# Performance work log

Measured on AMD Instinct MI355X. Metric: run time of the kernel, lower is better.

## Reference

```python
import jax, jax.numpy as jnp
import numpy as np

HEADS, HID, OUT_C, IN_C = 8, 128, 2, 64
D = HID // HEADS
NODE = {"cell0": 50000, "cell1": 100000, "cell2": 25000}
# (src_type, dst_type, edge_name, num_edges)
ETYPES = [("cell0", "cell0", "u00", 200000),
          ("cell1", "cell1", "u11", 200000),
          ("cell1", "cell0", "b10", 100000),
          ("cell2", "cell1", "b21", 50000)]


def _segment_softmax(scores, seg, num_segments):
    # numerically-stable softmax over irregular destination segments
    m = jax.ops.segment_max(scores, seg, num_segments=num_segments)
    e = jnp.exp(scores - m[seg])
    s = jax.ops.segment_sum(e, seg, num_segments=num_segments)
    return e / (s[seg] + 1e-16)


def setup_inputs() -> dict:
    key = jax.random.key(0)
    ks = iter(jax.random.split(key, 64))
    s = 0.1
    inp = {}
    for nt, n in NODE.items():
        inp[f"x_{nt}"] = jax.random.normal(next(ks), (n, IN_C), jnp.float32)
    for st, dt, name, e in ETYPES:
        src = jax.random.randint(next(ks), (e,), 0, NODE[st], jnp.int32)
        dst = jax.random.randint(next(ks), (e,), 0, NODE[dt], jnp.int32)
        inp[f"ei_{name}"] = jnp.stack([src, dst])
    # HANConv params: per node-type projection, per edge-type attention vectors
    for nt in NODE:
        inp[f"W_{nt}"] = jax.random.normal(next(ks), (IN_C, HID), jnp.float32) * s
        inp[f"b_{nt}"] = jnp.zeros((HID,), jnp.float32)
    for _, _, name, _ in ETYPES:
        inp[f"as_{name}"] = jax.random.normal(next(ks), (HEADS, D), jnp.float32) * s
        inp[f"ad_{name}"] = jax.random.normal(next(ks), (HEADS, D), jnp.float32) * s
    # semantic attention params + final classifier
    inp["k_w"] = jax.random.normal(next(ks), (HID, HID), jnp.float32) * s
    inp["k_b"] = jnp.zeros((HID,), jnp.float32)
    inp["q"] = jax.random.normal(next(ks), (HID,), jnp.float32) * s
    inp["lin_w"] = jax.random.normal(next(ks), (HID, OUT_C), jnp.float32) * s
    inp["lin_b"] = jnp.zeros((OUT_C,), jnp.float32)
    return inp


def _han_conv(x, ei, W, b, att_s, att_d, k_w, k_b, q):
    # node-level: project each node type -> [N, H, D]
    h = {nt: (x[nt] @ W[nt] + b[nt]).reshape(-1, HEADS, D) for nt in NODE}
    outs = {nt: [] for nt in NODE}
    for st, dt, name, _ in ETYPES:
        xs, xd = h[st], h[dt]
        a_s = (xs * att_s[name]).sum(-1)  # [Ns, H]
        a_d = (xd * att_d[name]).sum(-1)  # [Nd, H]
        src, dst = ei[name][0], ei[name][1]
        alpha = jax.nn.leaky_relu(a_s[src] + a_d[dst], 0.2)  # [E, H]
        alpha = _segment_softmax(alpha, dst, NODE[dt])
        msg = xs[src] * alpha[:, :, None]  # [E, H, D]
        agg = jax.ops.segment_sum(msg, dst, num_segments=NODE[dt])
        outs[dt].append(jax.nn.relu(agg.reshape(-1, HID)))
    # semantic-level attention across metapaths per dst node type
    res = {}
    for nt, lst in outs.items():
        if not lst:
            res[nt] = None
            continue
        stk = jnp.stack(lst)  # [M, N, HID]
        score = (q * jnp.tanh(stk @ k_w + k_b).mean(1)).sum(-1)  # [M]
        attn = jax.nn.softmax(score)
        res[nt] = jnp.einsum('m,mnf->nf', attn, stk)
    return res


def reference(x_cell0, x_cell1, x_cell2,
              W_cell0, b_cell0, W_cell1, b_cell1, W_cell2, b_cell2,
              as_u00, ad_u00, as_u11, ad_u11, as_b10, ad_b10, as_b21, ad_b21,
              k_w, k_b, q, lin_w, lin_b,
              ei_u00, ei_u11, ei_b10, ei_b21):
    x = {"cell0": x_cell0, "cell1": x_cell1, "cell2": x_cell2}
    ei = {"u00": ei_u00, "u11": ei_u11, "b10": ei_b10, "b21": ei_b21}
    W = {"cell0": W_cell0, "cell1": W_cell1, "cell2": W_cell2}
    b = {"cell0": b_cell0, "cell1": b_cell1, "cell2": b_cell2}
    att_s = {"u00": as_u00, "u11": as_u11, "b10": as_b10, "b21": as_b21}
    att_d = {"u00": ad_u00, "u11": ad_u11, "b10": ad_b10, "b21": ad_b21}
    # HAN.forward calls han_conv twice with identical inputs (first result
    # discarded); in eval mode (dropout off) both calls are identical math,
    # so we compute it once.
    out = _han_conv(x, ei, W, b, att_s, att_d, k_w, k_b, q)
    pooled = sum(jnp.sum(v, axis=0) for v in out.values() if v is not None)  # global_add_pool, batch=None
    return jax.nn.sigmoid(pooled[None, :] @ lin_w + lin_b)  # [1, OUT_C]
```

## Files before the change

### kernel.cpp

```cpp
#include <hip/hip_runtime.h>
#include <hip/hip_fp16.h>

#define N0 50000
#define N1 100000
#define N2 25000
#define E00 200000
#define E11 200000
#define E10 100000
#define E21 50000
#define EE  550000
#define ND  300000
#define NB  293
#define NT_ALL 18750
#define HID 128
#define INC 64

typedef _Float16 half8 __attribute__((ext_vector_type(8)));
typedef _Float16 half4_t __attribute__((ext_vector_type(4)));
typedef float float4v __attribute__((ext_vector_type(4)));
typedef float floatx2 __attribute__((ext_vector_type(2)));

struct PrepT {
    const float* W; const float* bias;
    const float* av0; const float* av1; const float* av2; const float* av3;
    _Float16* wtg; _Float16* adtg; float* bdc;
};

__global__ __launch_bounds__(256) void prep_kernel(
    PrepT p0, PrepT p1, PrepT p2,
    const float* __restrict__ kw, const float* __restrict__ lw,
    unsigned char* __restrict__ kwf8)
{
    if (blockIdx.x >= 24) {
        int base = (blockIdx.x - 24) * 256 + threadIdx.x;
        for (int it = 0; it < 9; ++it) {
            int idx = base + it * 2048;
            int f = idx >> 7, g = idx & 127;
            float v;
            if (f < 128)      v = kw[g * 128 + f];
            else if (f < 130) v = lw[g * 2 + (f - 128)];
            else              v = 0.f;
            int r = __builtin_amdgcn_cvt_pk_fp8_f32(v, 0.f, 0, false);
            kwf8[idx] = (unsigned char)r;
        }
        return;
    }
    PrepT P = (blockIdx.x >= 16) ? p2 : (blockIdx.x >= 8) ? p1 : p0;
    const int lb = blockIdx.x & 7;
    const int t2 = lb * 256 + threadIdx.x;

    {
        int f = t2 >> 4, g0 = (t2 & 15) * 4;
        half4_t v;
#pragma unroll
        for (int j = 0; j < 4; ++j) v[j] = (_Float16)P.W[(g0 + j) * 128 + f];
        *(half4_t*)&P.wtg[f * 64 + g0] = v;
    }
    {
        int c = t2 >> 6, g = t2 & 63;
        const float* av = (c < 8) ? P.av0 : (c < 16) ? P.av1 : (c < 24) ? P.av2 : P.av3;
        float v = 0.f;
        if (av) {
            int hh = c & 7;
#pragma unroll
            for (int d = 0; d < 16; ++d)
                v += P.W[g * 128 + hh * 16 + d] * av[hh * 16 + d];
        }
        P.adtg[c * 64 + g] = (_Float16)v;
    }
    if (lb == 0 && threadIdx.x < 32) {
        int c = threadIdx.x;
        const float* av = (c < 8) ? P.av0 : (c < 16) ? P.av1 : (c < 24) ? P.av2 : P.av3;
        float v = 0.f;
        if (av) {
            int hh = c & 7;
#pragma unroll
            for (int d = 0; d < 16; ++d)
                v += P.bias[hh * 16 + d] * av[hh * 16 + d];
        }
        P.bdc[c] = v;
    }
}

struct PT {
    const float* x; const float* bias; unsigned char* h;
    float* ao0; float* ao1; float* ao2; float* ao3;
    const _Float16* wtg; const _Float16* adtg; const float* bdc;
    int N; int ntiles; int bstart; int nblocks;
};

#define HPAD 136

__global__ __launch_bounds__(256, 2) void proj_mfma(PT t0, PT t1, PT t2)
{
    __shared__ _Float16 ht[4][16][HPAD];
    const int tid = threadIdx.x;
    const int lane = tid & 63, wv = tid >> 6;
    const int fi = lane & 15, hi = lane >> 4;

    PT A = (blockIdx.x >= t2.bstart) ? t2 : (blockIdx.x >= t1.bstart) ? t1 : t0;

    half8 bfr[8][2], bd[2][2];
#pragma unroll
    for (int nt = 0; nt < 8; ++nt)
#pragma unroll
        for (int kb = 0; kb < 2; ++kb)
            bfr[nt][kb] = *(const half8*)&A.wtg[(nt * 16 + fi) * 64 + kb * 32 + hi * 8];
#pragma unroll
    for (int t = 0; t < 2; ++t)
#pragma unroll
        for (int kb = 0; kb < 2; ++kb)
            bd[t][kb] = *(const half8*)&A.adtg[(t * 16 + fi) * 64 + kb * 32 + hi * 8];

    float bvv[8];
#pragma unroll
    for (int nt = 0; nt < 8; ++nt) bvv[nt] = A.bias[nt * 16 + fi];
    const float bdc0 = A.bdc[fi];
    const float bdc1 = A.bdc[16 + fi];

    float* aolo = (fi >= 8) ? A.ao1 : A.ao0;
    float* aohi = (fi >= 8) ? A.ao3 : A.ao2;
    const bool has_hi = (A.ao2 != nullptr) || (A.ao3 != nullptr);

    const int stride = A.nblocks * 4;
    for (int t = (blockIdx.x - A.bstart) * 4 + wv; t < A.ntiles; t += stride) {
        const int base = t * 16;
        int rsrc = base + fi; if (rsrc >= A.N) rsrc = A.N - 1;
        const float* xp = A.x + (size_t)rsrc * 64 + hi * 8;
        float4 u0 = *(const float4*)(xp);
        float4 u1 = *(const float4*)(xp + 4);
        float4 u2 = *(const float4*)(xp + 32);
        float4 u3 = *(const float4*)(xp + 36);
        half8 a0, a1;
        a0[0] = (_Float16)u0.x; a0[1] = (_Float16)u0.y; a0[2] = (_Float16)u0.z; a0[3] = (_Float16)u0.w;
        a0[4] = (_Float16)u1.x; a0[5] = (_Float16)u1.y; a0[6] = (_Float16)u1.z; a0[7] = (_Float16)u1.w;
        a1[0] = (_Float16)u2.x; a1[1] = (_Float16)u2.y; a1[2] = (_Float16)u2.z; a1[3] = (_Float16)u2.w;
        a1[4] = (_Float16)u3.x; a1[5] = (_Float16)u3.y; a1[6] = (_Float16)u3.z; a1[7] = (_Float16)u3.w;

        float4v c[8];
#pragma unroll
        for (int nt = 0; nt < 8; ++nt) {
            float4v z = {0.f, 0.f, 0.f, 0.f};
            z = __builtin_amdgcn_mfma_f32_16x16x32_f16(a0, bfr[nt][0], z, 0, 0, 0);
            z = __builtin_amdgcn_mfma_f32_16x16x32_f16(a1, bfr[nt][1], z, 0, 0, 0);
            c[nt] = z;
        }
        float4v d0 = {0.f, 0.f, 0.f, 0.f};
        d0 = __builtin_amdgcn_mfma_f32_16x16x32_f16(a0, bd[0][0], d0, 0, 0, 0);
        d0 = __builtin_amdgcn_mfma_f32_16x16x32_f16(a1, bd[0][1], d0, 0, 0, 0);
        float4v d1 = {0.f, 0.f, 0.f, 0.f};
        if (has_hi) {
            d1 = __builtin_amdgcn_mfma_f32_16x16x32_f16(a0, bd[1][0], d1, 0, 0, 0);
            d1 = __builtin_amdgcn_mfma_f32_16x16x32_f16(a1, bd[1][1], d1, 0, 0, 0);
        }

#pragma unroll
        for (int nt = 0; nt < 8; ++nt)
#pragma unroll
            for (int r = 0; r < 4; ++r)
                ht[wv][hi * 4 + r][nt * 16 + fi] = (_Float16)(c[nt][r] + bvv[nt]);
#pragma unroll
        for (int i = 0; i < 4; ++i) {
            int row = i * 4 + hi;
            int node = base + row;
            if (node < A.N) {
                half8 v = *(const half8*)&ht[wv][row][fi * 8];
                int pa = __builtin_amdgcn_cvt_pk_fp8_f32((float)v[0], (float)v[1], 0, false);
                pa = __builtin_amdgcn_cvt_pk_fp8_f32((float)v[2], (float)v[3], pa, true);
                int pb = __builtin_amdgcn_cvt_pk_fp8_f32((float)v[4], (float)v[5], 0, false);
                pb = __builtin_amdgcn_cvt_pk_fp8_f32((float)v[6], (float)v[7], pb, true);
                int2 o = {pa, pb};
                *(int2*)(A.h + (size_t)node * 128 + fi * 8) = o;
            }
        }
        if (aolo) {
#pragma unroll
            for (int r = 0; r < 4; ++r) {
                int node = base + hi * 4 + r;
                if (node < A.N) aolo[(size_t)node * 8 + (fi & 7)] = d0[r] + bdc0;
            }
        }
        if (aohi) {
#pragma unroll
            for (int r = 0; r < 4; ++r) {
                int node = base + hi * 4 + r;
                if (node < A.N) aohi[(size_t)node * 8 + (fi & 7)] = d1[r] + bdc1;
            }
        }
    }
}

__device__ __forceinline__ void decode_edge(
    int e, const int* ei00, const int* ei10, const int* ei11, const int* ei21,
    int& src, int& slot)
{
    if (e < E00)                    { src = ei00[e];               slot = ei00[E00 + e]; }
    else if (e < E00 + E10)         { int i = e - E00;             src = ei10[i]; slot = 50000  + ei10[E10 + i]; }
    else if (e < E00 + E10 + E11)   { int i = e - E00 - E10;       src = ei11[i]; slot = 100000 + ei11[E11 + i]; }
    else                            { int i = e - E00 - E10 - E11; src = ei21[i]; slot = 200000 + ei21[E21 + i]; }
}

__global__ __launch_bounds__(256) void count_kernel(
    const int* __restrict__ ei00, const int* __restrict__ ei10,
    const int* __restrict__ ei11, const int* __restrict__ ei21,
    int* __restrict__ cnt)
{
    int e = blockIdx.x * 256 + threadIdx.x;
    if (e >= EE) return;
    int src, slot;
    decode_edge(e, ei00, ei10, ei11, ei21, src, slot);
    atomicAdd(&cnt[slot], 1);
}

__global__ __launch_bounds__(256) void scan1_kernel(
    const int* __restrict__ cnt, int* __restrict__ part)
{
    const int tid = threadIdx.x, b = blockIdx.x;
    int i0 = b * 1024 + tid * 4;
    int s = 0;
#pragma unroll
    for (int k = 0; k < 4; ++k) { int i = i0 + k; s += (i < ND) ? cnt[i] : 0; }
#pragma unroll
    for (int off = 1; off < 64; off <<= 1) s += __shfl_xor(s, off);
    __shared__ int wt[4];
    if ((tid & 63) == 0) wt[tid >> 6] = s;
    __syncthreads();
    if (tid == 0) part[b] = wt[0] + wt[1] + wt[2] + wt[3];
}

__global__ __launch_bounds__(256) void scan2_kernel(int* __restrict__ part)
{
    const int t = threadIdx.x;
    int p0 = (2 * t     < NB) ? part[2 * t]     : 0;
    int p1 = (2 * t + 1 < NB) ? part[2 * t + 1] : 0;
    int ps = p0 + p1;
    __shared__ int sd[256];
    sd[t] = ps; __syncthreads();
    for (int d = 1; d < 256; d <<= 1) {
        int v = (t >= d) ? sd[t - d] : 0;
        __syncthreads();
        sd[t] += v;
        __syncthreads();
    }
    int exc = sd[t] - ps;
    if (2 * t     < NB) part[2 * t]     = exc;
    if (2 * t + 1 < NB) part[2 * t + 1] = exc + p0;
}

__global__ __launch_bounds__(256) void scan3_kernel(
    const int* __restrict__ cnt, const int* __restrict__ part,
    int* __restrict__ off, int* __restrict__ cursor)
{
    const int tid = threadIdx.x, b = blockIdx.x;
    const int lane = tid & 63, wv = tid >> 6;
    int i0 = b * 1024 + tid * 4;
    int v[4];
#pragma unroll
    for (int k = 0; k < 4; ++k) { int i = i0 + k; v[k] = (i < ND) ? cnt[i] : 0; }
    int ts = v[0] + v[1] + v[2] + v[3];
    int inc = ts;
#pragma unroll
    for (int d = 1; d < 64; d <<= 1) {
        int u = __shfl_up(inc, d);
        if (lane >= d) inc += u;
    }
    int wexc = inc - ts;
    __shared__ int wt[4];
    if (lane == 63) wt[wv] = inc;
    __syncthreads();
    int wbase = 0;
    for (int w = 0; w < wv; ++w) wbase += wt[w];
    int base = part[b] + wbase + wexc;
    int pre = 0;
#pragma unroll
    for (int k = 0; k < 4; ++k) {
        int i = i0 + k;
        if (i < ND) { off[i] = base + pre; cursor[i] = base + pre; }
        pre += v[k];
    }
}

__global__ __launch_bounds__(256) void fill_kernel(
    const int* __restrict__ ei00, const int* __restrict__ ei10,
    const int* __restrict__ ei11, const int* __restrict__ ei21,
    const float* __restrict__ as00, const float* __restrict__ ad00,
    const float* __restrict__ as10, const float* __restrict__ ad10,
    const float* __restrict__ as11, const float* __restrict__ ad11,
    const float* __restrict__ as21, const float* __restrict__ ad21,
    int* __restrict__ cursor, int* __restrict__ srcs, _Float16* __restrict__ wgt)
{
    int e = blockIdx.x * 256 + threadIdx.x;
    if (e >= EE) return;
    int src, d, slot;
    const float* asp; const float* adp;
    if (e < E00) {
        src = ei00[e]; d = ei00[E00 + e]; slot = d; asp = as00; adp = ad00;
    } else if (e < E00 + E10) {
        int i = e - E00; src = ei10[i]; d = ei10[E10 + i]; slot = 50000 + d; asp = as10; adp = ad10;
    } else if (e < E00 + E10 + E11) {
        int i = e - E00 - E10; src = ei11[i]; d = ei11[E11 + i]; slot = 100000 + d; asp = as11; adp = ad11;
    } else {
        int i = e - E00 - E10 - E11; src = ei21[i]; d = ei21[E21 + i]; slot = 200000 + d; asp = as21; adp = ad21;
    }
    float4 sa0 = *(const float4*)(asp + (size_t)src * 8);
    float4 sa1 = *(const float4*)(asp + (size_t)src * 8 + 4);
    float4 da0 = *(const float4*)(adp + (size_t)d * 8);
    float4 da1 = *(const float4*)(adp + (size_t)d * 8 + 4);
    float vv[8] = {sa0.x + da0.x, sa0.y + da0.y, sa0.z + da0.z, sa0.w + da0.w,
                   sa1.x + da1.x, sa1.y + da1.y, sa1.z + da1.z, sa1.w + da1.w};
    half8 w;
#pragma unroll
    for (int h = 0; h < 8; ++h) {
        float v = vv[h];
        v = v > 0.f ? v : 0.2f * v;
        w[h] = (_Float16)__expf(v);
    }
    int pos = atomicAdd(&cursor[slot], 1);
    srcs[pos] = src;
    *(half8*)(wgt + (size_t)pos * 8) = w;
}

__global__ __launch_bounds__(256) void gather_kernel(
    const int* __restrict__ cnt, const int* __restrict__ off,
    const int* __restrict__ srcs, const _Float16* __restrict__ wgt,
    const unsigned char* __restrict__ h0, const unsigned char* __restrict__ h1,
    const unsigned char* __restrict__ h2,
    unsigned char* __restrict__ agg)
{
    const int gid = blockIdx.x * 256 + threadIdx.x;
    const int lane = gid & 63;
    const int grp = lane >> 4, lg = lane & 15;
    const int slot = (gid >> 6) * 4 + grp;
    const int head = lg >> 1;
    const unsigned char* hs = (slot < 50000) ? h0 : (slot < 200000) ? h1 : h2;
    const int deg = cnt[slot], st = off[slot];

    int degm = deg;
    degm = max(degm, __shfl_xor(degm, 16));
    degm = max(degm, __shfl_xor(degm, 32));

    float acc[8] = {0.f, 0.f, 0.f, 0.f, 0.f, 0.f, 0.f, 0.f};
    float sw = 0.f;
    int i = 0;
    for (; i + 2 <= degm; i += 2) {
        bool a0 = (i < deg), a1 = (i + 1 < deg);
        int s0 = 0, s1 = 0;
        if (a0) s0 = srcs[st + i];
        if (a1) s1 = srcs[st + i + 1];
        float w0 = 0.f, w1 = 0.f;
        unsigned long long v0 = 0, v1 = 0;
        if (a0) { w0 = (float)wgt[(size_t)(st + i) * 8 + head];
                  v0 = *(const unsigned long long*)(hs + (size_t)s0 * 128 + lg * 8); }
        if (a1) { w1 = (float)wgt[(size_t)(st + i + 1) * 8 + head];
                  v1 = *(const unsigned long long*)(hs + (size_t)s1 * 128 + lg * 8); }
        int l0 = (int)(v0 & 0xffffffffu), m0 = (int)(v0 >> 32);
        int l1 = (int)(v1 & 0xffffffffu), m1 = (int)(v1 >> 32);
        floatx2 f0a = __builtin_amdgcn_cvt_pk_f32_fp8(l0, false);
        floatx2 f0b = __builtin_amdgcn_cvt_pk_f32_fp8(l0, true);
        floatx2 f0c = __builtin_amdgcn_cvt_pk_f32_fp8(m0, false);
        floatx2 f0d = __builtin_amdgcn_cvt_pk_f32_fp8(m0, true);
        floatx2 f1a = __builtin_amdgcn_cvt_pk_f32_fp8(l1, false);
        floatx2 f1b = __builtin_amdgcn_cvt_pk_f32_fp8(l1, true);
        floatx2 f1c = __builtin_amdgcn_cvt_pk_f32_fp8(m1, false);
        floatx2 f1d = __builtin_amdgcn_cvt_pk_f32_fp8(m1, true);
        acc[0] += w0 * f0a.x + w1 * f1a.x;
        acc[1] += w0 * f0a.y + w1 * f1a.y;
        acc[2] += w0 * f0b.x + w1 * f1b.x;
        acc[3] += w0 * f0b.y + w1 * f1b.y;
        acc[4] += w0 * f0c.x + w1 * f1c.x;
        acc[5] += w0 * f0c.y + w1 * f1c.y;
        acc[6] += w0 * f0d.x + w1 * f1d.x;
        acc[7] += w0 * f0d.y + w1 * f1d.y;
        sw += w0 + w1;
    }
    if (i < degm) {
        bool a0 = (i < deg);
        int s0 = 0;
        if (a0) s0 = srcs[st + i];
        float w0 = 0.f;
        unsigned long long v0 = 0;
        if (a0) { w0 = (float)wgt[(size_t)(st + i) * 8 + head];
                  v0 = *(const unsigned long long*)(hs + (size_t)s0 * 128 + lg * 8); }
        int l0 = (int)(v0 & 0xffffffffu), m0 = (int)(v0 >> 32);
        floatx2 f0a = __builtin_amdgcn_cvt_pk_f32_fp8(l0, false);
        floatx2 f0b = __builtin_amdgcn_cvt_pk_f32_fp8(l0, true);
        floatx2 f0c = __builtin_amdgcn_cvt_pk_f32_fp8(m0, false);
        floatx2 f0d = __builtin_amdgcn_cvt_pk_f32_fp8(m0, true);
        acc[0] += w0 * f0a.x; acc[1] += w0 * f0a.y;
        acc[2] += w0 * f0b.x; acc[3] += w0 * f0b.y;
        acc[4] += w0 * f0c.x; acc[5] += w0 * f0c.y;
        acc[6] += w0 * f0d.x; acc[7] += w0 * f0d.y;
        sw += w0;
    }

    float rr = __builtin_amdgcn_rcpf(sw + 1e-16f);
    float r[8];
#pragma unroll
    for (int j = 0; j < 8; ++j) r[j] = fmaxf(acc[j] * rr, 0.f);
    int pa = __builtin_amdgcn_cvt_pk_fp8_f32(r[0], r[1], 0, false);
    pa = __builtin_amdgcn_cvt_pk_fp8_f32(r[2], r[3], pa, true);
    int pb = __builtin_amdgcn_cvt_pk_fp8_f32(r[4], r[5], 0, false);
    pb = __builtin_amdgcn_cvt_pk_fp8_f32(r[6], r[7], pb, true);
    int2 o = {pa, pb};
    *(int2*)(agg + (size_t)slot * 128 + lg * 8) = o;
}

__global__ __launch_bounds__(256, 2) void semantic_kernel(
    const unsigned char* __restrict__ agg, const unsigned char* __restrict__ kwf8,
    const float* __restrict__ kb, const float* __restrict__ q,
    float* __restrict__ cs2, float* __restrict__ score)
{
    __shared__ float redv[12];
    const int tid = threadIdx.x;
    const int lane = tid & 63, wv = tid >> 6;
    const int fi = lane & 15, hi = lane >> 4;

    if (tid < 12) redv[tid] = 0.f;
    __syncthreads();

    long bf[9][4];
#pragma unroll
    for (int ft = 0; ft < 9; ++ft)
#pragma unroll
        for (int kk = 0; kk < 4; ++kk)
            bf[ft][kk] = *(const long*)&kwf8[(ft * 16 + fi) * 128 + kk * 32 + hi * 8];

    float qv[8], kbv[8];
#pragma unroll
    for (int ft = 0; ft < 8; ++ft) {
        qv[ft] = q[ft * 16 + fi];
        kbv[ft] = kb[ft * 16 + fi];
    }

    float sc[4] = {0.f, 0.f, 0.f, 0.f};
    float cs[4] = {0.f, 0.f, 0.f, 0.f};
    const int wid = blockIdx.x * 4 + wv;
    const int nw = gridDim.x * 4;

    long af[4] = {0, 0, 0, 0};
    int t = wid;
    if (t < NT_ALL) {
        const unsigned char* rowp = agg + ((size_t)(t * 16 + fi) * 128 + hi * 8);
        af[0] = *(const long*)(rowp);
        af[1] = *(const long*)(rowp + 32);
        af[2] = *(const long*)(rowp + 64);
        af[3] = *(const long*)(rowp + 96);
    }
    while (t < NT_ALL) {
        const int tn = t + nw;
        long afn[4] = {0, 0, 0, 0};
        if (tn < NT_ALL) {
            const unsigned char* rowp = agg + ((size_t)(tn * 16 + fi) * 128 + hi * 8);
            afn[0] = *(const long*)(rowp);
            afn[1] = *(const long*)(rowp + 32);
            afn[2] = *(const long*)(rowp + 64);
            afn[3] = *(const long*)(rowp + 96);
        }
        const int m = (t >= 12500) ? 3 : (t >= 6250) ? 2 : (t >= 3125) ? 1 : 0;
        float tsc = 0.f, tcs;
#pragma unroll
        for (int ft = 0; ft < 8; ++ft) {
            float4v c = {0.f, 0.f, 0.f, 0.f};
            c = __builtin_amdgcn_mfma_f32_16x16x32_fp8_fp8(af[0], bf[ft][0], c, 0, 0, 0);
            c = __builtin_amdgcn_mfma_f32_16x16x32_fp8_fp8(af[1], bf[ft][1], c, 0, 0, 0);
            c = __builtin_amdgcn_mfma_f32_16x16x32_fp8_fp8(af[2], bf[ft][2], c, 0, 0, 0);
            c = __builtin_amdgcn_mfma_f32_16x16x32_fp8_fp8(af[3], bf[ft][3], c, 0, 0, 0);
#pragma unroll
            for (int r = 0; r < 4; ++r) {
                float y = c[r] + kbv[ft];
                float e = __expf(2.f * y);
                tsc += qv[ft] * (1.f - 2.f * __builtin_amdgcn_rcpf(e + 1.f));
            }
        }
        {
            float4v c = {0.f, 0.f, 0.f, 0.f};
            c = __builtin_amdgcn_mfma_f32_16x16x32_fp8_fp8(af[0], bf[8][0], c, 0, 0, 0);
            c = __builtin_amdgcn_mfma_f32_16x16x32_fp8_fp8(af[1], bf[8][1], c, 0, 0, 0);
            c = __builtin_amdgcn_mfma_f32_16x16x32_fp8_fp8(af[2], bf[8][2], c, 0, 0, 0);
            c = __builtin_amdgcn_mfma_f32_16x16x32_fp8_fp8(af[3], bf[8][3], c, 0, 0, 0);
            tcs = c[0] + c[1] + c[2] + c[3];
        }
        if (m == 0)      { sc[0] += tsc; cs[0] += tcs; }
        else if (m == 1) { sc[1] += tsc; cs[1] += tcs; }
        else if (m == 2) { sc[2] += tsc; cs[2] += tcs; }
        else             { sc[3] += tsc; cs[3] += tcs; }
        t = tn;
        af[0] = afn[0]; af[1] = afn[1]; af[2] = afn[2]; af[3] = afn[3];
    }

#pragma unroll
    for (int m = 0; m < 4; ++m) {
        float s = sc[m];
#pragma unroll
        for (int off = 1; off < 64; off <<= 1) s += __shfl_xor(s, off);
        if (lane == 0 && s != 0.f) atomicAdd(&redv[m], s);
        float v = cs[m];
        v += __shfl_xor(v, 16);
        v += __shfl_xor(v, 32);
        if (hi == 0 && fi < 2 && v != 0.f) atomicAdd(&redv[4 + 2 * m + fi], v);
    }
    __syncthreads();
    if (tid < 4)              atomicAdd(&score[tid], redv[tid]);
    if (tid >= 4 && tid < 12) atomicAdd(&cs2[tid - 4], redv[tid]);
}

__global__ void final_kernel(const float* __restrict__ cs2,
                             const float* __restrict__ score,
                             const float* __restrict__ lb,
                             float* __restrict__ out)
{
    float s0 = score[0] / (float)N0;
    float s1 = score[1] / (float)N0;
    float s2 = score[2] / (float)N1;
    float s3 = score[3] / (float)N1;
    float m0 = fmaxf(s0, s1);
    float e0 = expf(s0 - m0), e1 = expf(s1 - m0);
    float a0 = e0 / (e0 + e1), a1 = e1 / (e0 + e1);
    float m1 = fmaxf(s2, s3);
    float e2 = expf(s2 - m1), e3 = expf(s3 - m1);
    float a2 = e2 / (e2 + e3), a3 = e3 / (e2 + e3);
    float z0 = a0 * cs2[0] + a1 * cs2[2] + a2 * cs2[4] + a3 * cs2[6] + lb[0];
    float z1 = a0 * cs2[1] + a1 * cs2[3] + a2 * cs2[5] + a3 * cs2[7] + lb[1];
    out[0] = 1.f / (1.f + expf(-z0));
    out[1] = 1.f / (1.f + expf(-z1));
}

extern "C" void kernel_launch(void* const* d_in, const int* in_sizes, int n_in,
                              void* d_out, int out_size, void* d_ws, size_t ws_size,
                              hipStream_t stream)
{
    const float* x0  = (const float*)d_in[0];
    const float* x1  = (const float*)d_in[1];
    const float* x2  = (const float*)d_in[2];
    const int* ei00  = (const int*)d_in[3];
    const int* ei11  = (const int*)d_in[4];
    const int* ei10  = (const int*)d_in[5];
    const int* ei21  = (const int*)d_in[6];
    const float* W0  = (const float*)d_in[7];  const float* b0 = (const float*)d_in[8];
    const float* W1  = (const float*)d_in[9];  const float* b1 = (const float*)d_in[10];
    const float* W2  = (const float*)d_in[11]; const float* b2 = (const float*)d_in[12];
    const float* as00 = (const float*)d_in[13]; const float* ad00 = (const float*)d_in[14];
    const float* as11 = (const float*)d_in[15]; const float* ad11 = (const float*)d_in[16];
    const float* as10 = (const float*)d_in[17]; const float* ad10 = (const float*)d_in[18];
    const float* as21 = (const float*)d_in[19]; const float* ad21 = (const float*)d_in[20];
    const float* kw  = (const float*)d_in[21]; const float* kb  = (const float*)d_in[22];
    const float* q   = (const float*)d_in[23];
    const float* lw  = (const float*)d_in[24]; const float* lb  = (const float*)d_in[25];
    float* out = (float*)d_out;

    char* p = (char*)d_ws;
    auto alloc = [&](size_t bytes) {
        char* r = p;
        p += (bytes + 255) & ~(size_t)255;
        return r;
    };
    unsigned char* h0 = (unsigned char*)alloc((size_t)N0 * 128);
    unsigned char* h1 = (unsigned char*)alloc((size_t)N1 * 128);
    unsigned char* h2 = (unsigned char*)alloc((size_t)N2 * 128);
    float* o_as00 = (float*)alloc((size_t)N0 * 32);
    float* o_ad00 = (float*)alloc((size_t)N0 * 32);
    float* o_as11 = (float*)alloc((size_t)N1 * 32);
    float* o_ad11 = (float*)alloc((size_t)N1 * 32);
    float* o_as10 = (float*)alloc((size_t)N1 * 32);
    float* o_ad10 = (float*)alloc((size_t)N0 * 32);
    float* o_as21 = (float*)alloc((size_t)N2 * 32);
    float* o_ad21 = (float*)alloc((size_t)N1 * 32);
    int* off    = (int*)alloc((size_t)ND * 4);
    int* cursor = (int*)alloc((size_t)ND * 4);
    int* part   = (int*)alloc((size_t)512 * 4);
    int* srcs   = (int*)alloc((size_t)EE * 4);
    _Float16* wgt = (_Float16*)alloc((size_t)EE * 16);
    unsigned char* agg = (unsigned char*)alloc((size_t)ND * 128);
    _Float16* wtg0 = (_Float16*)alloc(128 * 64 * 2);
    _Float16* wtg1 = (_Float16*)alloc(128 * 64 * 2);
    _Float16* wtg2 = (_Float16*)alloc(128 * 64 * 2);
    _Float16* adtg0 = (_Float16*)alloc(32 * 64 * 2);
    _Float16* adtg1 = (_Float16*)alloc(32 * 64 * 2);
    _Float16* adtg2 = (_Float16*)alloc(32 * 64 * 2);
    float* bdcg = (float*)alloc(3 * 32 * 4);
    unsigned char* kwf8 = (unsigned char*)alloc(144 * 128);
    char* zstart = p;
    int* cnt = (int*)alloc((size_t)ND * 4);
    float* colsum2 = (float*)alloc(8 * 4);
    float* score   = (float*)alloc(4 * 4);
    size_t zbytes = (size_t)(p - zstart);

    (void)hipMemsetAsync(zstart, 0, zbytes, stream);

    PrepT pp0 = {W0, b0, as00, ad00, ad10, nullptr, wtg0, adtg0, bdcg + 0};
    PrepT pp1 = {W1, b1, as11, ad11, as10, ad21,    wtg1, adtg1, bdcg + 32};
    PrepT pp2 = {W2, b2, as21, nullptr, nullptr, nullptr, wtg2, adtg2, bdcg + 64};
    prep_kernel<<<32, 256, 0, stream>>>(pp0, pp1, pp2, kw, lw, kwf8);

    PT t0 = {x0, b0, h0,
             o_as00, o_ad00, o_ad10, nullptr,
             wtg0, adtg0, bdcg + 0,
             N0, 3125, 0, 296};
    PT t1 = {x1, b1, h1,
             o_as11, o_ad11, o_as10, o_ad21,
             wtg1, adtg1, bdcg + 32,
             N1, 6250, 296, 584};
    PT t2 = {x2, b2, h2,
             o_as21, nullptr, nullptr, nullptr,
             wtg2, adtg2, bdcg + 64,
             N2, 1563, 880, 144};
    proj_mfma<<<1024, 256, 0, stream>>>(t0, t1, t2);

    count_kernel<<<(EE + 255) / 256, 256, 0, stream>>>(ei00, ei10, ei11, ei21, cnt);
    scan1_kernel<<<NB, 256, 0, stream>>>(cnt, part);
    scan2_kernel<<<1, 256, 0, stream>>>(part);
    scan3_kernel<<<NB, 256, 0, stream>>>(cnt, part, off, cursor);
    fill_kernel<<<(EE + 255) / 256, 256, 0, stream>>>(ei00, ei10, ei11, ei21,
        o_as00, o_ad00, o_as10, o_ad10, o_as11, o_ad11, o_as21, o_ad21,
        cursor, srcs, wgt);

    gather_kernel<<<ND / 16, 256, 0, stream>>>(cnt, off, srcs, wgt, h0, h1, h2, agg);

    semantic_kernel<<<1024, 256, 0, stream>>>(agg, kwf8, kb, q, colsum2, score);

    final_kernel<<<1, 1, 0, stream>>>(colsum2, score, lb, out);
}
```

Baseline: 289.3 us.

## Fuse CSR build launches into neighbors and widen gather to 16-byte rows

Result: faster. 283.1 us (-2.2%).

```diff
diff --git a/kernel.cpp b/kernel.cpp
--- a/kernel.cpp
+++ b/kernel.cpp
@@ -26,11 +26,32 @@
     _Float16* wtg; _Float16* adtg; float* bdc;
 };
 
+__device__ __forceinline__ void decode_edge(
+    int e, const int* ei00, const int* ei10, const int* ei11, const int* ei21,
+    int& src, int& slot)
+{
+    if (e < E00)                    { src = ei00[e];               slot = ei00[E00 + e]; }
+    else if (e < E00 + E10)         { int i = e - E00;             src = ei10[i]; slot = 50000  + ei10[E10 + i]; }
+    else if (e < E00 + E10 + E11)   { int i = e - E00 - E10;       src = ei11[i]; slot = 100000 + ei11[E11 + i]; }
+    else                            { int i = e - E00 - E10 - E11; src = ei21[i]; slot = 200000 + ei21[E21 + i]; }
+}
+
 __global__ __launch_bounds__(256) void prep_kernel(
     PrepT p0, PrepT p1, PrepT p2,
     const float* __restrict__ kw, const float* __restrict__ lw,
-    unsigned char* __restrict__ kwf8)
-{
+    unsigned char* __restrict__ kwf8,
+    const int* __restrict__ ei00, const int* __restrict__ ei10,
+    const int* __restrict__ ei11, const int* __restrict__ ei21,
+    int* __restrict__ cnt)
+{
+    if (blockIdx.x >= 32) {
+        int e = (blockIdx.x - 32) * 256 + threadIdx.x;
+        if (e >= EE) return;
+        int src, slot;
+        decode_edge(e, ei00, ei10, ei11, ei21, src, slot);
+        atomicAdd(&cnt[slot], 1);
+        return;
+    }
     if (blockIdx.x >= 24) {
         int base = (blockIdx.x - 24) * 256 + threadIdx.x;
         for (int it = 0; it < 9; ++it) {
@@ -48,7 +69,6 @@
     PrepT P = (blockIdx.x >= 16) ? p2 : (blockIdx.x >= 8) ? p1 : p0;
     const int lb = blockIdx.x & 7;
     const int t2 = lb * 256 + threadIdx.x;
-
     {
         int f = t2 >> 4, g0 = (t2 & 15) * 4;
         half4_t v;
@@ -90,13 +110,31 @@
 };
 
 #define HPAD 136
-
-__global__ __launch_bounds__(256, 2) void proj_mfma(PT t0, PT t1, PT t2)
+#define PROJ_BLKS 1024
+
+__global__ __launch_bounds__(256, 2) void proj_mfma(
+    PT t0, PT t1, PT t2,
+    const int* __restrict__ cnt, int* __restrict__ part)
 {
     __shared__ _Float16 ht[4][16][HPAD];
+    __shared__ int swt[4];
     const int tid = threadIdx.x;
     const int lane = tid & 63, wv = tid >> 6;
     const int fi = lane & 15, hi = lane >> 4;
+
+    if (blockIdx.x >= PROJ_BLKS) {
+        const int b = blockIdx.x - PROJ_BLKS;
+        int i0 = b * 1024 + tid * 4;
+        int s = 0;
+#pragma unroll
+        for (int k = 0; k < 4; ++k) { int i = i0 + k; s += (i < ND) ? cnt[i] : 0; }
+#pragma unroll
+        for (int off = 1; off < 64; off <<= 1) s += __shfl_xor(s, off);
+        if ((tid & 63) == 0) swt[tid >> 6] = s;
+        __syncthreads();
+        if (tid == 0) part[b] = swt[0] + swt[1] + swt[2] + swt[3];
+        return;
+    }
 
     PT A = (blockIdx.x >= t2.bstart) ? t2 : (blockIdx.x >= t1.bstart) ? t1 : t0;
 
@@ -190,69 +228,31 @@
     }
 }
 
-__device__ __forceinline__ void decode_edge(
-    int e, const int* ei00, const int* ei10, const int* ei11, const int* ei21,
-    int& src, int& slot)
-{
-    if (e < E00)                    { src = ei00[e];               slot = ei00[E00 + e]; }
-    else if (e < E00 + E10)         { int i = e - E00;             src = ei10[i]; slot = 50000  + ei10[E10 + i]; }
-    else if (e < E00 + E10 + E11)   { int i = e - E00 - E10;       src = ei11[i]; slot = 100000 + ei11[E11 + i]; }
-    else                            { int i = e - E00 - E10 - E11; src = ei21[i]; slot = 200000 + ei21[E21 + i]; }
-}
-
-__global__ __launch_bounds__(256) void count_kernel(
-    const int* __restrict__ ei00, const int* __restrict__ ei10,
-    const int* __restrict__ ei11, const int* __restrict__ ei21,
-    int* __restrict__ cnt)
-{
-    int e = blockIdx.x * 256 + threadIdx.x;
-    if (e >= EE) return;
-    int src, slot;
-    decode_edge(e, ei00, ei10, ei11, ei21, src, slot);
-    atomicAdd(&cnt[slot], 1);
-}
-
-__global__ __launch_bounds__(256) void scan1_kernel(
-    const int* __restrict__ cnt, int* __restrict__ part)
-{
-    const int tid = threadIdx.x, b = blockIdx.x;
-    int i0 = b * 1024 + tid * 4;
-    int s = 0;
-#pragma unroll
-    for (int k = 0; k < 4; ++k) { int i = i0 + k; s += (i < ND) ? cnt[i] : 0; }
-#pragma unroll
-    for (int off = 1; off < 64; off <<= 1) s += __shfl_xor(s, off);
-    __shared__ int wt[4];
-    if ((tid & 63) == 0) wt[tid >> 6] = s;
-    __syncthreads();
-    if (tid == 0) part[b] = wt[0] + wt[1] + wt[2] + wt[3];
-}
-
-__global__ __launch_bounds__(256) void scan2_kernel(int* __restrict__ part)
-{
-    const int t = threadIdx.x;
-    int p0 = (2 * t     < NB) ? part[2 * t]     : 0;
-    int p1 = (2 * t + 1 < NB) ? part[2 * t + 1] : 0;
-    int ps = p0 + p1;
-    __shared__ int sd[256];
-    sd[t] = ps; __syncthreads();
-    for (int d = 1; d < 256; d <<= 1) {
-        int v = (t >= d) ? sd[t - d] : 0;
-        __syncthreads();
-        sd[t] += v;
-        __syncthreads();
-    }
-    int exc = sd[t] - ps;
-    if (2 * t     < NB) part[2 * t]     = exc;
-    if (2 * t + 1 < NB) part[2 * t + 1] = exc + p0;
-}
-
-__global__ __launch_bounds__(256) void scan3_kernel(
+__global__ __launch_bounds__(256) void scan23_kernel(
     const int* __restrict__ cnt, const int* __restrict__ part,
     int* __restrict__ off, int* __restrict__ cursor)
 {
+    __shared__ int sd[256];
+    __shared__ int pex[512];
+    __shared__ int wt[4];
     const int tid = threadIdx.x, b = blockIdx.x;
     const int lane = tid & 63, wv = tid >> 6;
+
+    int p0 = (2 * tid     < NB) ? part[2 * tid]     : 0;
+    int p1 = (2 * tid + 1 < NB) ? part[2 * tid + 1] : 0;
+    int ps = p0 + p1;
+    sd[tid] = ps; __syncthreads();
+    for (int d = 1; d < 256; d <<= 1) {
+        int v = (tid >= d) ? sd[tid - d] : 0;
+        __syncthreads();
+        sd[tid] += v;
+        __syncthreads();
+    }
+    int exc = sd[tid] - ps;
+    pex[2 * tid] = exc;
+    pex[2 * tid + 1] = exc + p0;
+    __syncthreads();
+
     int i0 = b * 1024 + tid * 4;
     int v[4];
 #pragma unroll
@@ -265,12 +265,11 @@
         if (lane >= d) inc += u;
     }
     int wexc = inc - ts;
-    __shared__ int wt[4];
     if (lane == 63) wt[wv] = inc;
     __syncthreads();
     int wbase = 0;
     for (int w = 0; w < wv; ++w) wbase += wt[w];
-    int base = part[b] + wbase + wexc;
+    int base = pex[b] + wbase + wexc;
     int pre = 0;
 #pragma unroll
     for (int k = 0; k < 4; ++k) {
@@ -329,18 +328,21 @@
 {
     const int gid = blockIdx.x * 256 + threadIdx.x;
     const int lane = gid & 63;
-    const int grp = lane >> 4, lg = lane & 15;
-    const int slot = (gid >> 6) * 4 + grp;
-    const int head = lg >> 1;
+    const int g8 = lane >> 3, sub = lane & 7;
+    const int slot = (gid >> 6) * 8 + g8;
     const unsigned char* hs = (slot < 50000) ? h0 : (slot < 200000) ? h1 : h2;
     const int deg = cnt[slot], st = off[slot];
 
     int degm = deg;
+    degm = max(degm, __shfl_xor(degm, 8));
     degm = max(degm, __shfl_xor(degm, 16));
     degm = max(degm, __shfl_xor(degm, 32));
 
-    float acc[8] = {0.f, 0.f, 0.f, 0.f, 0.f, 0.f, 0.f, 0.f};
+    float acc[16];
+#pragma unroll
+    for (int j = 0; j < 16; ++j) acc[j] = 0.f;
     float sw = 0.f;
+
     int i = 0;
     for (; i + 2 <= degm; i += 2) {
         bool a0 = (i < deg), a1 = (i + 1 < deg);
@@ -348,29 +350,24 @@
         if (a0) s0 = srcs[st + i];
         if (a1) s1 = srcs[st + i + 1];
         float w0 = 0.f, w1 = 0.f;
-        unsigned long long v0 = 0, v1 = 0;
-        if (a0) { w0 = (float)wgt[(size_t)(st + i) * 8 + head];
-                  v0 = *(const unsigned long long*)(hs + (size_t)s0 * 128 + lg * 8); }
-        if (a1) { w1 = (float)wgt[(size_t)(st + i + 1) * 8 + head];
-                  v1 = *(const unsigned long long*)(hs + (size_t)s1 * 128 + lg * 8); }
-        int l0 = (int)(v0 & 0xffffffffu), m0 = (int)(v0 >> 32);
-        int l1 = (int)(v1 & 0xffffffffu), m1 = (int)(v1 >> 32);
-        floatx2 f0a = __builtin_amdgcn_cvt_pk_f32_fp8(l0, false);
-        floatx2 f0b = __builtin_amdgcn_cvt_pk_f32_fp8(l0, true);
-        floatx2 f0c = __builtin_amdgcn_cvt_pk_f32_fp8(m0, false);
-        floatx2 f0d = __builtin_amdgcn_cvt_pk_f32_fp8(m0, true);
-        floatx2 f1a = __builtin_amdgcn_cvt_pk_f32_fp8(l1, false);
-        floatx2 f1b = __builtin_amdgcn_cvt_pk_f32_fp8(l1, true);
-        floatx2 f1c = __builtin_amdgcn_cvt_pk_f32_fp8(m1, false);
-        floatx2 f1d = __builtin_amdgcn_cvt_pk_f32_fp8(m1, true);
-        acc[0] += w0 * f0a.x + w1 * f1a.x;
-        acc[1] += w0 * f0a.y + w1 * f1a.y;
-        acc[2] += w0 * f0b.x + w1 * f1b.x;
-        acc[3] += w0 * f0b.y + w1 * f1b.y;
-        acc[4] += w0 * f0c.x + w1 * f1c.x;
-        acc[5] += w0 * f0c.y + w1 * f1c.y;
-        acc[6] += w0 * f0d.x + w1 * f1d.x;
-        acc[7] += w0 * f0d.y + w1 * f1d.y;
+        int4 v0 = {0, 0, 0, 0}, v1 = {0, 0, 0, 0};
+        if (a0) { w0 = (float)wgt[(size_t)(st + i) * 8 + sub];
+                  v0 = *(const int4*)(hs + (size_t)s0 * 128 + sub * 16); }
+        if (a1) { w1 = (float)wgt[(size_t)(st + i + 1) * 8 + sub];
+                  v1 = *(const int4*)(hs + (size_t)s1 * 128 + sub * 16); }
+        const int wa[4] = {v0.x, v0.y, v0.z, v0.w};
+        const int wb[4] = {v1.x, v1.y, v1.z, v1.w};
+#pragma unroll
+        for (int k = 0; k < 4; ++k) {
+            floatx2 fa0 = __builtin_amdgcn_cvt_pk_f32_fp8(wa[k], false);
+            floatx2 fa1 = __builtin_amdgcn_cvt_pk_f32_fp8(wa[k], true);
+            floatx2 fb0 = __builtin_amdgcn_cvt_pk_f32_fp8(wb[k], false);
+            floatx2 fb1 = __builtin_amdgcn_cvt_pk_f32_fp8(wb[k], true);
+            acc[4 * k + 0] += w0 * fa0.x + w1 * fb0.x;
+            acc[4 * k + 1] += w0 * fa0.y + w1 * fb0.y;
+            acc[4 * k + 2] += w0 * fa1.x + w1 * fb1.x;
+            acc[4 * k + 3] += w0 * fa1.y + w1 * fb1.y;
+        }
         sw += w0 + w1;
     }
     if (i < degm) {
@@ -378,37 +375,45 @@
         int s0 = 0;
         if (a0) s0 = srcs[st + i];
         float w0 = 0.f;
-        unsigned long long v0 = 0;
-        if (a0) { w0 = (float)wgt[(size_t)(st + i) * 8 + head];
-                  v0 = *(const unsigned long long*)(hs + (size_t)s0 * 128 + lg * 8); }
-        int l0 = (int)(v0 & 0xffffffffu), m0 = (int)(v0 >> 32);
-        floatx2 f0a = __builtin_amdgcn_cvt_pk_f32_fp8(l0, false);
-        floatx2 f0b = __builtin_amdgcn_cvt_pk_f32_fp8(l0, true);
-        floatx2 f0c = __builtin_amdgcn_cvt_pk_f32_fp8(m0, false);
-        floatx2 f0d = __builtin_amdgcn_cvt_pk_f32_fp8(m0, true);
-        acc[0] += w0 * f0a.x; acc[1] += w0 * f0a.y;
-        acc[2] += w0 * f0b.x; acc[3] += w0 * f0b.y;
-        acc[4] += w0 * f0c.x; acc[5] += w0 * f0c.y;
-        acc[6] += w0 * f0d.x; acc[7] += w0 * f0d.y;
+        int4 v0 = {0, 0, 0, 0};
+        if (a0) { w0 = (float)wgt[(size_t)(st + i) * 8 + sub];
+                  v0 = *(const int4*)(hs + (size_t)s0 * 128 + sub * 16); }
+        const int wa[4] = {v0.x, v0.y, v0.z, v0.w};
+#pragma unroll
+        for (int k = 0; k < 4; ++k) {
+            floatx2 fa0 = __builtin_amdgcn_cvt_pk_f32_fp8(wa[k], false);
+            floatx2 fa1 = __builtin_amdgcn_cvt_pk_f32_fp8(wa[k], true);
+            acc[4 * k + 0] += w0 * fa0.x;
+            acc[4 * k + 1] += w0 * fa0.y;
+            acc[4 * k + 2] += w0 * fa1.x;
+            acc[4 * k + 3] += w0 * fa1.y;
+        }
         sw += w0;
     }
 
     float rr = __builtin_amdgcn_rcpf(sw + 1e-16f);
-    float r[8];
-#pragma unroll
-    for (int j = 0; j < 8; ++j) r[j] = fmaxf(acc[j] * rr, 0.f);
-    int pa = __builtin_amdgcn_cvt_pk_fp8_f32(r[0], r[1], 0, false);
-    pa = __builtin_amdgcn_cvt_pk_fp8_f32(r[2], r[3], pa, true);
-    int pb = __builtin_amdgcn_cvt_pk_fp8_f32(r[4], r[5], 0, false);
-    pb = __builtin_amdgcn_cvt_pk_fp8_f32(r[6], r[7], pb, true);
-    int2 o = {pa, pb};
-    *(int2*)(agg + (size_t)slot * 128 + lg * 8) = o;
+    int4 o;
+    int pk[4];
+#pragma unroll
+    for (int k = 0; k < 4; ++k) {
+        float r0 = fmaxf(acc[4 * k + 0] * rr, 0.f);
+        float r1 = fmaxf(acc[4 * k + 1] * rr, 0.f);
+        float r2 = fmaxf(acc[4 * k + 2] * rr, 0.f);
+        float r3 = fmaxf(acc[4 * k + 3] * rr, 0.f);
+        int p = __builtin_amdgcn_cvt_pk_fp8_f32(r0, r1, 0, false);
+        p = __builtin_amdgcn_cvt_pk_fp8_f32(r2, r3, p, true);
+        pk[k] = p;
+    }
+    o.x = pk[0]; o.y = pk[1]; o.z = pk[2]; o.w = pk[3];
+    *(int4*)(agg + (size_t)slot * 128 + sub * 16) = o;
 }
 
 __global__ __launch_bounds__(256, 2) void semantic_kernel(
     const unsigned char* __restrict__ agg, const unsigned char* __restrict__ kwf8,
     const float* __restrict__ kb, const float* __restrict__ q,
-    float* __restrict__ cs2, float* __restrict__ score)
+    const float* __restrict__ lb,
+    float* __restrict__ cs2, float* __restrict__ score,
+    unsigned int* __restrict__ done, float* __restrict__ out)
 {
     __shared__ float redv[12];
     const int tid = threadIdx.x;
@@ -502,27 +507,29 @@
     __syncthreads();
     if (tid < 4)              atomicAdd(&score[tid], redv[tid]);
     if (tid >= 4 && tid < 12) atomicAdd(&cs2[tid - 4], redv[tid]);
-}
-
-__global__ void final_kernel(const float* __restrict__ cs2,
-                             const float* __restrict__ score,
-                             const float* __restrict__ lb,
-                             float* __restrict__ out)
-{
-    float s0 = score[0] / (float)N0;
-    float s1 = score[1] / (float)N0;
-    float s2 = score[2] / (float)N1;
-    float s3 = score[3] / (float)N1;
-    float m0 = fmaxf(s0, s1);
-    float e0 = expf(s0 - m0), e1 = expf(s1 - m0);
-    float a0 = e0 / (e0 + e1), a1 = e1 / (e0 + e1);
-    float m1 = fmaxf(s2, s3);
-    float e2 = expf(s2 - m1), e3 = expf(s3 - m1);
-    float a2 = e2 / (e2 + e3), a3 = e3 / (e2 + e3);
-    float z0 = a0 * cs2[0] + a1 * cs2[2] + a2 * cs2[4] + a3 * cs2[6] + lb[0];
-    float z1 = a0 * cs2[1] + a1 * cs2[3] + a2 * cs2[5] + a3 * cs2[7] + lb[1];
-    out[0] = 1.f / (1.f + expf(-z0));
-    out[1] = 1.f / (1.f + expf(-z1));
+
+    __syncthreads();
+    if (tid == 0) {
+        __threadfence();
+        unsigned int old = atomicAdd(done, 1u);
+        if (old == gridDim.x - 1) {
+            __threadfence();
+            float s0 = score[0] / (float)N0;
+            float s1 = score[1] / (float)N0;
+            float s2 = score[2] / (float)N1;
+            float s3 = score[3] / (float)N1;
+            float m0 = fmaxf(s0, s1);
+            float e0 = __expf(s0 - m0), e1 = __expf(s1 - m0);
+            float a0 = e0 / (e0 + e1), a1 = e1 / (e0 + e1);
+            float m1 = fmaxf(s2, s3);
+            float e2 = __expf(s2 - m1), e3 = __expf(s3 - m1);
+            float a2 = e2 / (e2 + e3), a3 = e3 / (e2 + e3);
+            float z0 = a0 * cs2[0] + a1 * cs2[2] + a2 * cs2[4] + a3 * cs2[6] + lb[0];
+            float z1 = a0 * cs2[1] + a1 * cs2[3] + a2 * cs2[5] + a3 * cs2[7] + lb[1];
+            out[0] = 1.f / (1.f + __expf(-z0));
+            out[1] = 1.f / (1.f + __expf(-z1));
+        }
+    }
 }
 
 extern "C" void kernel_launch(void* const* d_in, const int* in_sizes, int n_in,
@@ -583,6 +590,7 @@
     int* cnt = (int*)alloc((size_t)ND * 4);
     float* colsum2 = (float*)alloc(8 * 4);
     float* score   = (float*)alloc(4 * 4);
+    unsigned int* done = (unsigned int*)alloc(4);
     size_t zbytes = (size_t)(p - zstart);
 
     (void)hipMemsetAsync(zstart, 0, zbytes, stream);
@@ -590,7 +598,8 @@
     PrepT pp0 = {W0, b0, as00, ad00, ad10, nullptr, wtg0, adtg0, bdcg + 0};
     PrepT pp1 = {W1, b1, as11, ad11, as10, ad21,    wtg1, adtg1, bdcg + 32};
     PrepT pp2 = {W2, b2, as21, nullptr, nullptr, nullptr, wtg2, adtg2, bdcg + 64};
-    prep_kernel<<<32, 256, 0, stream>>>(pp0, pp1, pp2, kw, lw, kwf8);
+    prep_kernel<<<32 + (EE + 255) / 256, 256, 0, stream>>>(
+        pp0, pp1, pp2, kw, lw, kwf8, ei00, ei10, ei11, ei21, cnt);
 
     PT t0 = {x0, b0, h0,
              o_as00, o_ad00, o_ad10, nullptr,
@@ -604,19 +613,16 @@
              o_as21, nullptr, nullptr, nullptr,
              wtg2, adtg2, bdcg + 64,
              N2, 1563, 880, 144};
-    proj_mfma<<<1024, 256, 0, stream>>>(t0, t1, t2);
-
-    count_kernel<<<(EE + 255) / 256, 256, 0, stream>>>(ei00, ei10, ei11, ei21, cnt);
-    scan1_kernel<<<NB, 256, 0, stream>>>(cnt, part);
-    scan2_kernel<<<1, 256, 0, stream>>>(part);
-    scan3_kernel<<<NB, 256, 0, stream>>>(cnt, part, off, cursor);
+    proj_mfma<<<PROJ_BLKS + NB, 256, 0, stream>>>(t0, t1, t2, cnt, part);
+
+    scan23_kernel<<<NB, 256, 0, stream>>>(cnt, part, off, cursor);
+
     fill_kernel<<<(EE + 255) / 256, 256, 0, stream>>>(ei00, ei10, ei11, ei21,
         o_as00, o_ad00, o_as10, o_ad10, o_as11, o_ad11, o_as21, o_ad21,
         cursor, srcs, wgt);
 
-    gather_kernel<<<ND / 16, 256, 0, stream>>>(cnt, off, srcs, wgt, h0, h1, h2, agg);
-
-    semantic_kernel<<<1024, 256, 0, stream>>>(agg, kwf8, kb, q, colsum2, score);
-
-    final_kernel<<<1, 1, 0, stream>>>(colsum2, score, lb, out);
-}
+    gather_kernel<<<ND / 32, 256, 0, stream>>>(cnt, off, srcs, wgt, h0, h1, h2, agg);
+
+    semantic_kernel<<<1024, 256, 0, stream>>>(agg, kwf8, kb, q, lb,
+                                              colsum2, score, done, out);
+}
```
